# Kernel tuning notes

Measured on AMD Instinct MI355X. Metric: run time of the kernel, lower is better.

Reference implementation:

```python
import jax, jax.numpy as jnp
import numpy as np

N_NODES = 100000
N_EDGES = 2000000
FEAT = 4
H = 64
L = 3  # num_mp_layers
E = 2  # edge_types


def _p(key, shape, scale=0.05):
    return jax.random.normal(key, shape, dtype=jnp.float32) * scale


def setup_inputs() -> dict:
    key = jax.random.key(0)
    ks = jax.random.split(key, 24)
    inp = {
        "x": jax.random.normal(ks[0], (N_NODES, FEAT), dtype=jnp.float32),
        "node_type": jax.random.randint(ks[1], (N_NODES,), 0, 3),
        "edge_index": jax.random.randint(ks[2], (2, N_EDGES), 0, N_NODES),
        "edge_type": jax.random.randint(ks[3], (N_EDGES,), 0, E),
        # input_proj: Linear(4,64) + LayerNorm(64)
        "in_w": _p(ks[4], (FEAT, H)), "in_b": _p(ks[5], (H,)),
        "ln_g": jnp.ones((H,), jnp.float32), "ln_b": jnp.zeros((H,), jnp.float32),
        # per-layer, per-edge-type message MLPs: Linear(2H,H) -> ReLU -> Linear(H,H)
        "mlp_w1": _p(ks[6], (L, E, 2 * H, H)), "mlp_b1": _p(ks[7], (L, E, H)),
        "mlp_w2": _p(ks[8], (L, E, H, H)), "mlp_b2": _p(ks[9], (L, E, H)),
        # per-layer GRUCell(H,H): gates ordered [r, z, n] as in torch
        "gru_wi": _p(ks[10], (L, H, 3 * H)), "gru_wh": _p(ks[11], (L, H, 3 * H)),
        "gru_bi": _p(ks[12], (L, 3 * H)), "gru_bh": _p(ks[13], (L, 3 * H)),
        # readout: Linear(H,H) -> ReLU -> Linear(H,1)
        "ro_w1": _p(ks[14], (H, H)), "ro_b1": _p(ks[15], (H,)),
        "ro_w2": _p(ks[16], (H, 1)), "ro_b2": _p(ks[17], (1,)),
    }
    return inp


def _layernorm(h, g, b, eps=1e-5):
    mu = jnp.mean(h, axis=-1, keepdims=True)
    var = jnp.mean(jnp.square(h - mu), axis=-1, keepdims=True)
    return (h - mu) * jax.lax.rsqrt(var + eps) * g + b


def _forward(x, edge_index, edge_type, node_type,
             in_w, in_b, ln_g, ln_b,
             mlp_w1, mlp_b1, mlp_w2, mlp_b2,
             gru_wi, gru_wh, gru_bi, gru_bh,
             ro_w1, ro_b1, ro_w2, ro_b2):
    n = x.shape[0]
    # input projection (dropout is identity at inference)
    h = jax.nn.relu(_layernorm(x @ in_w + in_b, ln_g, ln_b))
    src, dst = edge_index[0], edge_index[1]
    for l in range(L):
        # gather -> concat: (M, 2H)
        mi = jnp.concatenate([h[src], h[dst]], axis=1)
        msg = jnp.zeros((mi.shape[0], H), dtype=h.dtype)
        for e in range(E):
            m = jax.nn.relu(mi @ mlp_w1[l, e] + mlp_b1[l, e]) @ mlp_w2[l, e] + mlp_b2[l, e]
            msg = msg + jnp.where((edge_type == e)[:, None], m, jnp.zeros((), h.dtype))
        # scatter_add over destination nodes
        agg = jax.ops.segment_sum(msg, dst, num_segments=n)
        # GRUCell(agg, h), torch gate order [r, z, n]
        gi = agg @ gru_wi[l] + gru_bi[l]
        gh = h @ gru_wh[l] + gru_bh[l]
        i_r, i_z, i_n = jnp.split(gi, 3, axis=-1)
        h_r, h_z, h_n = jnp.split(gh, 3, axis=-1)
        r = jax.nn.sigmoid(i_r + h_r)
        z = jax.nn.sigmoid(i_z + h_z)
        nn_ = jnp.tanh(i_n + r * h_n)
        h = (1.0 - z) * nn_ + z * h
    out = jax.nn.relu(h @ ro_w1 + ro_b1) @ ro_w2 + ro_b2  # (N, 1)
    # additive correction for data qubits (node_type==0); other nodes zeroed
    corr = jnp.where(node_type == 0, x[:, 0] + out[:, 0], jnp.zeros((), x.dtype))
    return corr


def reference(x, node_type, edge_index, edge_type,
              in_w, in_b, ln_g, ln_b,
              mlp_w1, mlp_b1, mlp_w2, mlp_b2,
              gru_wi, gru_wh, gru_bi, gru_bh,
              ro_w1, ro_b1, ro_w2, ro_b2):
    return _forward(x, edge_index, edge_type, node_type,
                    in_w, in_b, ln_g, ln_b,
                    mlp_w1, mlp_b1, mlp_w2, mlp_b2,
                    gru_wi, gru_wh, gru_bi, gru_bh,
                    ro_w1, ro_b1, ro_w2, ro_b2)
```

## Files before the change

kernel.cpp:

```cpp
#include <hip/hip_runtime.h>

typedef unsigned int u32;
typedef unsigned short u16;
typedef unsigned long long u64;

using short8 = __attribute__((ext_vector_type(8))) short;
using f32x4  = __attribute__((ext_vector_type(4))) float;

__device__ __forceinline__ u32 f2bf(float f) {
    u32 u = __float_as_uint(f);
    return (u + 0x7fffu + ((u >> 16) & 1u)) >> 16;
}
__device__ __forceinline__ u32 pk(float a, float b) {
    return f2bf(a) | (f2bf(b) << 16);
}
__device__ __forceinline__ u32 f2bf_fast(float f) {
    return (__float_as_uint(f) + 0x8000u) >> 16;
}
__device__ __forceinline__ u32 pk_fast(float a, float b) {
    return f2bf_fast(a) | (f2bf_fast(b) << 16);
}
__device__ __forceinline__ float bflo(u32 u) { return __uint_as_float(u << 16); }
__device__ __forceinline__ float bfhi(u32 u) { return __uint_as_float(u & 0xffff0000u); }
__device__ __forceinline__ float bfu(u16 u) { return __uint_as_float(((u32)u) << 16); }

union U8 { u32 u[4]; short8 v; };

__global__ void k_input_proj(const float* __restrict__ x, const float* __restrict__ in_w,
                             const float* __restrict__ in_b, const float* __restrict__ ln_g,
                             const float* __restrict__ ln_b, u16* __restrict__ hbf,
                             float* __restrict__ agg, int n_nodes) {
    const int lane = threadIdx.x & 63;
    const int node = blockIdx.x * 4 + (threadIdx.x >> 6);
    if (node >= n_nodes) return;
    agg[(size_t)node * 64 + lane] = 0.f;
    float acc = in_b[lane];
#pragma unroll
    for (int k = 0; k < 4; ++k) acc = fmaf(x[node * 4 + k], in_w[k * 64 + lane], acc);
    float s = acc;
#pragma unroll
    for (int off = 32; off > 0; off >>= 1) s += __shfl_xor(s, off);
    float mu = s * (1.f / 64.f);
    float d = acc - mu;
    float vs = d * d;
#pragma unroll
    for (int off = 32; off > 0; off >>= 1) vs += __shfl_xor(vs, off);
    float inv = rsqrtf(vs * (1.f / 64.f) + 1e-5f);
    float hv = fmaxf(d * inv * ln_g[lane] + ln_b[lane], 0.f);
    hbf[(size_t)node * 64 + lane] = (u16)f2bf(hv);
}

__global__ void k_hist(const int* __restrict__ dst, const int* __restrict__ ety,
                       int* __restrict__ cnt, int* __restrict__ key, int M, int N) {
    int i = blockIdx.x * 256 + threadIdx.x;
    if (i < M) {
        int k = (ety[i] & 1) * N + dst[i];
        key[i] = k;
        atomicAdd(&cnt[k], 1);
    }
}

__global__ void k_scan1(int* __restrict__ data, int* __restrict__ part, int N) {
    __shared__ int s[1024];
    const int t = threadIdx.x;
    const int i = blockIdx.x * 1024 + t;
    int v = (i < N) ? data[i] : 0;
    s[t] = v;
    __syncthreads();
#pragma unroll
    for (int d = 1; d < 1024; d <<= 1) {
        int x = (t >= d) ? s[t - d] : 0;
        __syncthreads();
        s[t] += x;
        __syncthreads();
    }
    if (i < N) data[i] = s[t] - v;
    if (t == 1023) part[blockIdx.x] = s[1023];
}

__global__ void k_scan2(int* __restrict__ part, int nb) {
    const int l = threadIdx.x & 63;
    int base = 0;
    for (int s = 0; s < nb; s += 64) {
        int i = s + l;
        int orig = (i < nb) ? part[i] : 0;
        int x = orig;
#pragma unroll
        for (int off = 1; off < 64; off <<= 1) {
            int t = __shfl_up(x, off);
            if (l >= off) x += t;
        }
        if (i < nb) part[i] = base + x - orig;
        base += __shfl(x, 63);
    }
}

__global__ void k_scan3(int* __restrict__ data, const int* __restrict__ part, int N,
                        int saveIdx, int* __restrict__ slot) {
    int i = blockIdx.x * 1024 + threadIdx.x;
    if (i < N) {
        int v = data[i] + part[blockIdx.x];
        data[i] = v;
        if (i == saveIdx) slot[0] = v;
    }
}

__global__ void k_filldst(const int* __restrict__ off, int* __restrict__ dstP,
                          int NB, int N, int M) {
    int b = blockIdx.x * 256 + threadIdx.x;
    if (b >= NB) return;
    int s = off[b];
    int e = (b + 1 < NB) ? off[b + 1] : M;
    int d = (b >= N) ? b - N : b;
    for (int p = s; p < e; ++p) dstP[p] = d;
}

__global__ void k_scatter(const int* __restrict__ src, const int* __restrict__ key,
                          int* __restrict__ cursor, int* __restrict__ srcP,
                          int M, int N, int nd8) {
    const int g = blockIdx.x & 7;
    const int nb = gridDim.x >> 3;
    const int bi = blockIdx.x >> 3;
    for (int e = bi * 256 + threadIdx.x; e < M; e += nb * 256) {
        int k = key[e];
        int d = (k >= N) ? k - N : k;
        if (d / nd8 == g) {
            int pos = atomicAdd(&cursor[k], 1);
            srcP[pos] = src[e] & 0x3FFFFFFF;
        }
    }
}

__global__ __launch_bounds__(256, 2) void k_edge_mlp(
    const u16* __restrict__ hbf, const int* __restrict__ srcP, const int* __restrict__ dstP,
    const int* __restrict__ t0p, const float* __restrict__ w1, const float* __restrict__ b1,
    const float* __restrict__ w2, const float* __restrict__ b2,
    float* __restrict__ agg, int M) {
    __shared__ u16 sMsg[4][4864];

    const int tid = threadIdx.x;
    const int l = tid & 63, wv = tid >> 6;
    const int l15 = l & 15, quad = l >> 4;
    const f32x4 vz = {0.f, 0.f, 0.f, 0.f};

    const int T0 = *t0p;
    const int half = gridDim.x >> 1;
    const int ty = (blockIdx.x >= half) ? 1 : 0;
    const int bi = ty ? (int)blockIdx.x - half : (int)blockIdx.x;

    const int n_tiles = (M + 63) >> 6;
    const int tlo = ty ? (T0 >> 6) : 0;
    const int thi = ty ? n_tiles : ((T0 + 63) >> 6);
    const int lo = ty ? T0 : 0;
    const int hi = ty ? M : T0;
    const int range = thi - tlo;
    const int per = (range + half - 1) / half;
    const int c0 = tlo + bi * per;
    const int c1 = min(c0 + per, thi);

    short8 Bf1[4][4], Bf2[2][4];
    float b1p[4][4], b2r[4];
#pragma unroll
    for (int ni = 0; ni < 4; ++ni) {
        const int c = ni * 16 + l15;
        b2r[ni] = b2[ty * 64 + c];
#pragma unroll
        for (int r = 0; r < 4; ++r) b1p[ni][r] = b1[ty * 64 + ni * 16 + quad * 4 + r];
#pragma unroll
        for (int s = 0; s < 4; ++s) {
            U8 tmp;
            const float* wp = w1 + (size_t)ty * 8192 + (size_t)(s * 32 + quad * 8) * 64 + c;
#pragma unroll
            for (int jp = 0; jp < 4; ++jp) tmp.u[jp] = pk(wp[(2 * jp) * 64], wp[(2 * jp + 1) * 64]);
            Bf1[s][ni] = tmp.v;
        }
#pragma unroll
        for (int s = 0; s < 2; ++s) {
            U8 tmp;
#pragma unroll
            for (int w = 0; w < 4; ++w) {
                const int row = s * 32 + (w >> 1) * 16 + quad * 4 + (w & 1) * 2;
                const float* wp = w2 + (size_t)ty * 4096 + (size_t)row * 64 + c;
                tmp.u[w] = pk(wp[0], wp[64]);
            }
            Bf2[s][ni] = tmp.v;
        }
    }

    u16* msg = sMsg[wv];

    int t = c0 + wv;
    int mdc = -1;
    int msn = 0, mdn = -1;
    short8 a1[4][4];
    if (t < c1) {
        int ec = min((t << 6) + l, M - 1);
        int ms = srcP[ec];
        mdc = dstP[ec];
#pragma unroll
        for (int mi = 0; mi < 4; ++mi) {
            int rs = __shfl(ms, mi * 16 + l15);
            int rd = __shfl(mdc, mi * 16 + l15);
#pragma unroll
            for (int s = 0; s < 4; ++s) {
                const int row = (s < 2) ? rs : rd;
                a1[mi][s] = *(const short8*)(hbf + (size_t)row * 64 + (s & 1) * 32 + quad * 8);
            }
        }
        int ecn = min(((t + 4) << 6) + l, M - 1);
        msn = srcP[ecn];
        mdn = dstP[ecn];
    }

    for (; t < c1; t += 4) {
        const int base = t << 6;
        const int ecf = min(((t + 8) << 6) + l, M - 1);
        const int msf = srcP[ecf];
        const int mdf = dstP[ecf];

#pragma unroll
        for (int mi = 0; mi < 4; ++mi) {
            f32x4 acc[4] = {vz, vz, vz, vz};
#pragma unroll
            for (int s = 0; s < 4; ++s)
#pragma unroll
                for (int ni = 0; ni < 4; ++ni)
                    acc[ni] = __builtin_amdgcn_mfma_f32_16x16x32_bf16(Bf1[s][ni], a1[mi][s], acc[ni], 0, 0, 0);
            {
                int rs = __shfl(msn, mi * 16 + l15);
                int rd = __shfl(mdn, mi * 16 + l15);
#pragma unroll
                for (int s = 0; s < 4; ++s) {
                    const int row = (s < 2) ? rs : rd;
                    a1[mi][s] = *(const short8*)(hbf + (size_t)row * 64 + (s & 1) * 32 + quad * 8);
                }
            }
            U8 pa, pb;
#pragma unroll
            for (int ni = 0; ni < 2; ++ni) {
                float h0 = fmaxf(acc[ni][0] + b1p[ni][0], 0.f);
                float h1 = fmaxf(acc[ni][1] + b1p[ni][1], 0.f);
                float h2 = fmaxf(acc[ni][2] + b1p[ni][2], 0.f);
                float h3 = fmaxf(acc[ni][3] + b1p[ni][3], 0.f);
                pa.u[ni * 2] = pk_fast(h0, h1);
                pa.u[ni * 2 + 1] = pk_fast(h2, h3);
            }
#pragma unroll
            for (int ni = 0; ni < 2; ++ni) {
                float h0 = fmaxf(acc[2 + ni][0] + b1p[2 + ni][0], 0.f);
                float h1 = fmaxf(acc[2 + ni][1] + b1p[2 + ni][1], 0.f);
                float h2 = fmaxf(acc[2 + ni][2] + b1p[2 + ni][2], 0.f);
                float h3 = fmaxf(acc[2 + ni][3] + b1p[2 + ni][3], 0.f);
                pb.u[ni * 2] = pk_fast(h0, h1);
                pb.u[ni * 2 + 1] = pk_fast(h2, h3);
            }
#pragma unroll
            for (int ni = 0; ni < 4; ++ni) {
                f32x4 tt = __builtin_amdgcn_mfma_f32_16x16x32_bf16(pa.v, Bf2[0][ni], vz, 0, 0, 0);
                f32x4 m2 = __builtin_amdgcn_mfma_f32_16x16x32_bf16(pb.v, Bf2[1][ni], tt, 0, 0, 0);
                const int c = ni * 16 + l15;
                const int e0 = mi * 16 + quad * 4;
                const float bb = b2r[ni];
                uint2 w;
                w.x = pk_fast(m2[0] + bb, m2[1] + bb);
                w.y = pk_fast(m2[2] + bb, m2[3] + bb);
                *(uint2*)(msg + c * 76 + e0) = w;
            }
        }

        {
            int eg = base + l;
            int dvz = (eg >= lo && eg < hi) ? mdc : -1;
            int dprev = __shfl_up(dvz, 1);
            u64 mask = __ballot((l == 0) || (dvz != dprev));
            float a = 0.f;
#pragma unroll
            for (int i = 0; i < 64; i += 4) {
                uint2 pr = *(const uint2*)(msg + l * 76 + i);
                float v0 = bflo(pr.x), v1 = bfhi(pr.x), v2 = bflo(pr.y), v3 = bfhi(pr.y);
#define RR_STEP(ii, vv)                                                         \
                a += (vv);                                                      \
                if ((ii) == 63 || ((mask >> ((ii) + 1)) & 1ull)) {              \
                    int dd = __builtin_amdgcn_readlane(dvz, (ii));              \
                    if (dd >= 0) unsafeAtomicAdd(agg + (size_t)dd * 64 + l, a); \
                    a = 0.f;                                                    \
                }
                RR_STEP(i, v0)
                RR_STEP(i + 1, v1)
                RR_STEP(i + 2, v2)
                RR_STEP(i + 3, v3)
#undef RR_STEP
            }
        }
        mdc = mdn;
        msn = msf;
        mdn = mdf;
    }
}

__global__ __launch_bounds__(256, 2) void k_gru_gemm(
    float* __restrict__ agg, u16* __restrict__ hbf,
    const float* __restrict__ wi, const float* __restrict__ wh,
    const float* __restrict__ bi, const float* __restrict__ bh, int n_nodes, int last,
    const float* __restrict__ ro_w1, const float* __restrict__ ro_b1,
    const float* __restrict__ ro_w2, const float* __restrict__ ro_b2,
    const float* __restrict__ x, const int* __restrict__ node_type, float* __restrict__ out) {
    extern __shared__ u16 smem[];
    u16* sRZ = smem;
    u16* sIN = smem + 128 * 136;
    u16* sHN = sIN + 64 * 72;
    u16* sTR = sHN + 64 * 72;
    u16* sRO = sTR + 4 * 16 * 72;

    const int tid = threadIdx.x;
    const int l = tid & 63, wv = tid >> 6;
    const int l15 = l & 15, quad = l >> 4;
    const f32x4 vz = {0.f, 0.f, 0.f, 0.f};

    for (int u = tid; u < 128 * 64; u += 256) {
        int c = u & 127, k0 = (u >> 7) * 2;
        float v0 = (k0 < 64) ? wi[k0 * 192 + c] : wh[(k0 - 64) * 192 + c];
        float v1 = (k0 < 64) ? wi[(k0 + 1) * 192 + c] : wh[(k0 + 1 - 64) * 192 + c];
        *(u32*)(sRZ + c * 136 + k0) = pk(v0, v1);
    }
    for (int u = tid; u < 64 * 32; u += 256) {
        int c = u & 63, k0 = (u >> 6) * 2;
        *(u32*)(sIN + c * 72 + k0) = pk(wi[k0 * 192 + 128 + c], wi[(k0 + 1) * 192 + 128 + c]);
        *(u32*)(sHN + c * 72 + k0) = pk(wh[k0 * 192 + 128 + c], wh[(k0 + 1) * 192 + 128 + c]);
        *(u32*)(sRO + c * 72 + k0) = pk(ro_w1[k0 * 64 + c], ro_w1[(k0 + 1) * 64 + c]);
    }
    float bR[4], bZ[4], bI[4], bH[4], b1v[4], w2v[4];
#pragma unroll
    for (int nt = 0; nt < 4; ++nt) {
        int j = nt * 16 + l15;
        bR[nt] = bi[j] + bh[j];
        bZ[nt] = bi[64 + j] + bh[64 + j];
        bI[nt] = bi[128 + j];
        bH[nt] = bh[128 + j];
        b1v[nt] = ro_b1[j];
        w2v[nt] = ro_w2[j];
    }
    const float b2s = ro_b2[0];
    __syncthreads();

    u16* tr = sTR + wv * (16 * 72);
    const f32x4 z4 = {0.f, 0.f, 0.f, 0.f};
    const int n_tiles = (n_nodes + 15) >> 4;
    const int g = blockIdx.x & 7, jb = blockIdx.x >> 3, nbg = gridDim.x >> 3;
    const int per8 = (n_tiles + 7) >> 3;
    const int glo = g * per8, ghi = min(glo + per8, n_tiles);
    for (int tile = glo + jb * 4 + wv; tile < ghi; tile += nbg * 4) {
        const int nb = tile << 4;
        const int arow = nb + l15;
        const int rowc = (arow < n_nodes) ? arow : (n_nodes - 1);
        short8 aA[2], aH[2];
#pragma unroll
        for (int s = 0; s < 2; ++s) {
            const float* ap = agg + (size_t)rowc * 64 + s * 32 + quad * 8;
            U8 tt;
#pragma unroll
            for (int jp = 0; jp < 4; ++jp) tt.u[jp] = pk(ap[2 * jp], ap[2 * jp + 1]);
            aA[s] = tt.v;
            aH[s] = *(const short8*)(hbf + (size_t)rowc * 64 + s * 32 + quad * 8);
        }
        if (!last && arow < n_nodes) {
#pragma unroll
            for (int s = 0; s < 2; ++s) {
                *(f32x4*)(agg + (size_t)rowc * 64 + s * 32 + quad * 8) = z4;
                *(f32x4*)(agg + (size_t)rowc * 64 + s * 32 + quad * 8 + 4) = z4;
            }
        }
        f32x4 D[16];
#pragma unroll
        for (int i = 0; i < 16; ++i) D[i] = vz;
#pragma unroll
        for (int nt = 0; nt < 8; ++nt) {
            const u16* bp = sRZ + (nt * 16 + l15) * 136 + quad * 8;
            D[nt] = __builtin_amdgcn_mfma_f32_16x16x32_bf16(aA[0], *(const short8*)bp, D[nt], 0, 0, 0);
            D[nt] = __builtin_amdgcn_mfma_f32_16x16x32_bf16(aA[1], *(const short8*)(bp + 32), D[nt], 0, 0, 0);
            D[nt] = __builtin_amdgcn_mfma_f32_16x16x32_bf16(aH[0], *(const short8*)(bp + 64), D[nt], 0, 0, 0);
            D[nt] = __builtin_amdgcn_mfma_f32_16x16x32_bf16(aH[1], *(const short8*)(bp + 96), D[nt], 0, 0, 0);
        }
#pragma unroll
        for (int nt = 0; nt < 4; ++nt) {
            const u16* ip = sIN + (nt * 16 + l15) * 72 + quad * 8;
            D[8 + nt] = __builtin_amdgcn_mfma_f32_16x16x32_bf16(aA[0], *(const short8*)ip, D[8 + nt], 0, 0, 0);
            D[8 + nt] = __builtin_amdgcn_mfma_f32_16x16x32_bf16(aA[1], *(const short8*)(ip + 32), D[8 + nt], 0, 0, 0);
            const u16* hp = sHN + (nt * 16 + l15) * 72 + quad * 8;
            D[12 + nt] = __builtin_amdgcn_mfma_f32_16x16x32_bf16(aH[0], *(const short8*)hp, D[12 + nt], 0, 0, 0);
            D[12 + nt] = __builtin_amdgcn_mfma_f32_16x16x32_bf16(aH[1], *(const short8*)(hp + 32), D[12 + nt], 0, 0, 0);
        }
#pragma unroll
        for (int nt = 0; nt < 4; ++nt) {
            const int j = nt * 16 + l15;
#pragma unroll
            for (int r = 0; r < 4; ++r) {
                const int nd = nb + quad * 4 + r;
                float rsv = D[nt][r] + bR[nt];
                float zsv = D[4 + nt][r] + bZ[nt];
                float inv = D[8 + nt][r] + bI[nt];
                float hnv = D[12 + nt][r] + bH[nt];
                float rr = 1.f / (1.f + __expf(-rsv));
                float zz = 1.f / (1.f + __expf(-zsv));
                float nn = tanhf(fmaf(rr, hnv, inv));
                float hv = (nd < n_nodes) ? bfu(hbf[(size_t)nd * 64 + j]) : 0.f;
                float nh = (1.f - zz) * nn + zz * hv;
                tr[(quad * 4 + r) * 72 + j] = (u16)f2bf(nh);
            }
        }
        {
            const int nd = nb + (l >> 2);
            if (nd < n_nodes) {
                const u16* sp = tr + (l >> 2) * 72 + (l & 3) * 16;
                uint4 va = *(const uint4*)sp;
                uint4 vb = *(const uint4*)(sp + 8);
                u16* dp = hbf + (size_t)nd * 64 + (l & 3) * 16;
                *(uint4*)dp = va;
                *(uint4*)(dp + 8) = vb;
            }
        }
        if (last) {
            short8 ar0 = *(const short8*)(tr + l15 * 72 + quad * 8);
            short8 ar1 = *(const short8*)(tr + l15 * 72 + 32 + quad * 8);
            float p[4] = {0.f, 0.f, 0.f, 0.f};
#pragma unroll
            for (int nt = 0; nt < 4; ++nt) {
                const u16* bp = sRO + (nt * 16 + l15) * 72 + quad * 8;
                f32x4 acc = __builtin_amdgcn_mfma_f32_16x16x32_bf16(ar0, *(const short8*)bp, vz, 0, 0, 0);
                acc = __builtin_amdgcn_mfma_f32_16x16x32_bf16(ar1, *(const short8*)(bp + 32), acc, 0, 0, 0);
#pragma unroll
                for (int r = 0; r < 4; ++r)
                    p[r] += fmaxf(acc[r] + b1v[nt], 0.f) * w2v[nt];
            }
#pragma unroll
            for (int off = 1; off < 16; off <<= 1)
#pragma unroll
                for (int r = 0; r < 4; ++r) p[r] += __shfl_xor(p[r], off);
            if (l15 == 0) {
#pragma unroll
                for (int r = 0; r < 4; ++r) {
                    const int nd = nb + quad * 4 + r;
                    if (nd < n_nodes) {
                        float o = p[r] + b2s;
                        out[nd] = (node_type[nd] == 0) ? (x[nd * 4] + o) : 0.f;
                    }
                }
            }
        }
    }
}

extern "C" void kernel_launch(void* const* d_in, const int* in_sizes, int n_in, void* d_out,
                              int out_size, void* d_ws, size_t ws_size, hipStream_t stream) {
    const float* x = (const float*)d_in[0];
    const int* node_type = (const int*)d_in[1];
    const int* edge_index = (const int*)d_in[2];
    const int* edge_type = (const int*)d_in[3];
    const float* in_w = (const float*)d_in[4];
    const float* in_b = (const float*)d_in[5];
    const float* ln_g = (const float*)d_in[6];
    const float* ln_b = (const float*)d_in[7];
    const float* mlp_w1 = (const float*)d_in[8];
    const float* mlp_b1 = (const float*)d_in[9];
    const float* mlp_w2 = (const float*)d_in[10];
    const float* mlp_b2 = (const float*)d_in[11];
    const float* gru_wi = (const float*)d_in[12];
    const float* gru_wh = (const float*)d_in[13];
    const float* gru_bi = (const float*)d_in[14];
    const float* gru_bh = (const float*)d_in[15];
    const float* ro_w1 = (const float*)d_in[16];
    const float* ro_b1 = (const float*)d_in[17];
    const float* ro_w2 = (const float*)d_in[18];
    const float* ro_b2 = (const float*)d_in[19];

    const int N = in_sizes[1];
    const int M = in_sizes[3];
    const int* src = edge_index;
    const int* dst = edge_index + M;

    char* wsb = (char*)d_ws;
    float* agg = (float*)wsb;
    u16* hbf = (u16*)(wsb + (size_t)N * 256);
    int* off = (int*)(wsb + (size_t)N * 384);
    int* part = (int*)(wsb + (size_t)N * 384 + (size_t)2 * N * 4);
    int* srcP = (int*)(wsb + (size_t)N * 384 + (size_t)2 * N * 4 + 4096);
    int* dstP = srcP + M;
    int* key = dstP + M;
    int* t0slot = part + 1000;

    const int NB = 2 * N;
    const int nb = (NB + 1023) / 1024;
    const int nd8 = (N + 7) / 8;

    hipMemsetAsync(off, 0, (size_t)NB * sizeof(int), stream);
    k_hist<<<(M + 255) / 256, 256, 0, stream>>>(dst, edge_type, off, key, M, N);
    k_scan1<<<nb, 1024, 0, stream>>>(off, part, NB);
    k_scan2<<<1, 64, 0, stream>>>(part, nb);
    k_scan3<<<nb, 1024, 0, stream>>>(off, part, NB, N, t0slot);
    k_filldst<<<(NB + 255) / 256, 256, 0, stream>>>(off, dstP, NB, N, M);
    k_scatter<<<2048, 256, 0, stream>>>(src, key, off, srcP, M, N, nd8);

    k_input_proj<<<(N + 3) / 4, 256, 0, stream>>>(x, in_w, in_b, ln_g, ln_b, hbf, agg, N);
    const size_t gruLds =
        (size_t)(128 * 136 + 64 * 72 + 64 * 72 + 4 * 16 * 72 + 64 * 72) * sizeof(u16);
    for (int l = 0; l < 3; ++l) {
        k_edge_mlp<<<1024, 256, 0, stream>>>(hbf, srcP, dstP, t0slot,
                                             mlp_w1 + (size_t)l * 2 * 128 * 64,
                                             mlp_b1 + (size_t)l * 2 * 64,
                                             mlp_w2 + (size_t)l * 2 * 64 * 64,
                                             mlp_b2 + (size_t)l * 2 * 64, agg, M);
        k_gru_gemm<<<1024, 256, gruLds, stream>>>(agg, hbf, gru_wi + (size_t)l * 64 * 192,
                                                  gru_wh + (size_t)l * 64 * 192,
                                                  gru_bi + (size_t)l * 192, gru_bh + (size_t)l * 192,
                                                  N, (l == 2) ? 1 : 0,
                                                  ro_w1, ro_b1, ro_w2, ro_b2,
                                                  x, node_type, (float*)d_out);
    }
}
```

Measured before the change: 760.8 us.

## Partition edge-MLP and input-proj work by XCD-aligned destination-node ranges

Edge tiles for each edge type are now split into 8 groups by destination-node range, and block index mod 8 picks the group. Since blocks are dispatched round-robin across the 8 XCDs, each XCD's L2 holds a contiguous slice of agg. The input projection uses the same grouping, and edge_mlp launch bounds rise to 4 waves per SIMD to allow more occupancy. This risks load imbalance between groups and register spilling from the tighter launch bound.

```diff
diff --git a/kernel.cpp b/kernel.cpp
--- a/kernel.cpp
+++ b/kernel.cpp
@@ -29,10 +29,11 @@
 __global__ void k_input_proj(const float* __restrict__ x, const float* __restrict__ in_w,
                              const float* __restrict__ in_b, const float* __restrict__ ln_g,
                              const float* __restrict__ ln_b, u16* __restrict__ hbf,
-                             float* __restrict__ agg, int n_nodes) {
+                             float* __restrict__ agg, int n_nodes, int nd8) {
     const int lane = threadIdx.x & 63;
-    const int node = blockIdx.x * 4 + (threadIdx.x >> 6);
-    if (node >= n_nodes) return;
+    const int g = blockIdx.x & 7, ib = blockIdx.x >> 3;
+    const int node = g * nd8 + ib * 4 + (threadIdx.x >> 6);
+    if (node >= n_nodes || node >= (g + 1) * nd8) return;
     agg[(size_t)node * 64 + lane] = 0.f;
     float acc = in_b[lane];
 #pragma unroll
@@ -131,11 +132,11 @@
     }
 }
 
-__global__ __launch_bounds__(256, 2) void k_edge_mlp(
+__global__ __launch_bounds__(256, 4) void k_edge_mlp(
     const u16* __restrict__ hbf, const int* __restrict__ srcP, const int* __restrict__ dstP,
     const int* __restrict__ t0p, const float* __restrict__ w1, const float* __restrict__ b1,
     const float* __restrict__ w2, const float* __restrict__ b2,
-    float* __restrict__ agg, int M) {
+    float* __restrict__ agg, int M, const int* __restrict__ offEnd, int N, int nd8) {
     __shared__ u16 sMsg[4][4864];
 
     const int tid = threadIdx.x;
@@ -146,15 +147,24 @@
     const int T0 = *t0p;
     const int half = gridDim.x >> 1;
     const int ty = (blockIdx.x >= half) ? 1 : 0;
-    const int bi = ty ? (int)blockIdx.x - half : (int)blockIdx.x;
-
-    const int n_tiles = (M + 63) >> 6;
-    const int tlo = ty ? (T0 >> 6) : 0;
-    const int thi = ty ? n_tiles : ((T0 + 63) >> 6);
-    const int lo = ty ? T0 : 0;
-    const int hi = ty ? M : T0;
+    const int sub = ty ? (int)blockIdx.x - half : (int)blockIdx.x;
+    const int g = sub & 7;
+    const int bi = sub >> 3;
+    const int nbg = half >> 3;
+
+    const int tyStart = ty ? T0 : 0;
+    const int tyEnd = ty ? M : T0;
+    const int k0 = g * nd8, k1 = (g + 1) * nd8;
+    const int b0 = (k0 == 0) ? tyStart : ((k0 >= N) ? tyEnd : offEnd[ty * N + k0 - 1]);
+    const int b1e = (k1 >= N) ? tyEnd : offEnd[ty * N + k1 - 1];
+
+    const int n_tiles_ty = (tyEnd + 63) >> 6;
+    const int tlo = b0 >> 6;
+    const int thi = (k1 >= N) ? n_tiles_ty : (b1e >> 6);
+    const int lo = tyStart;
+    const int hi = tyEnd;
     const int range = thi - tlo;
-    const int per = (range + half - 1) / half;
+    const int per = (range + nbg - 1) / nbg;
     const int c0 = tlo + bi * per;
     const int c1 = min(c0 + per, thi);
 
@@ -500,7 +510,7 @@
     k_filldst<<<(NB + 255) / 256, 256, 0, stream>>>(off, dstP, NB, N, M);
     k_scatter<<<2048, 256, 0, stream>>>(src, key, off, srcP, M, N, nd8);
 
-    k_input_proj<<<(N + 3) / 4, 256, 0, stream>>>(x, in_w, in_b, ln_g, ln_b, hbf, agg, N);
+    k_input_proj<<<8 * ((nd8 + 3) / 4), 256, 0, stream>>>(x, in_w, in_b, ln_g, ln_b, hbf, agg, N, nd8);
     const size_t gruLds =
         (size_t)(128 * 136 + 64 * 72 + 64 * 72 + 4 * 16 * 72 + 64 * 72) * sizeof(u16);
     for (int l = 0; l < 3; ++l) {
@@ -508,7 +518,7 @@
                                              mlp_w1 + (size_t)l * 2 * 128 * 64,
                                              mlp_b1 + (size_t)l * 2 * 64,
                                              mlp_w2 + (size_t)l * 2 * 64 * 64,
-                                             mlp_b2 + (size_t)l * 2 * 64, agg, M);
+                                             mlp_b2 + (size_t)l * 2 * 64, agg, M, off, N, nd8);
         k_gru_gemm<<<1024, 256, gruLds, stream>>>(agg, hbf, gru_wi + (size_t)l * 64 * 192,
                                                   gru_wh + (size_t)l * 64 * 192,
                                                   gru_bi + (size_t)l * 192, gru_bh + (size_t)l * 192,
```

After: 1.727 ms. 127% more time.
